# Optimization experiments

Hardware: AMD Instinct MI355X
Metric: run time of the kernel (lower is better)

The kernel has to match this reference:

```python
import jax, jax.numpy as jnp
import numpy as np

B, D, L, E, RH, EH = 8192, 1024, 3, 8, 128, 256  # batch, dim, levels, experts, router hidden, expert hidden


def setup_inputs() -> dict:
    key = jax.random.key(0)
    ks = jax.random.split(key, 9)
    s_d = 1.0 / np.sqrt(D)
    s_rh = 1.0 / np.sqrt(RH)
    s_eh = 1.0 / np.sqrt(EH)
    return {
        "x": jax.random.normal(ks[0], (B, D), dtype=jnp.float32),
        # routers: Linear(D,128) -> ReLU -> Linear(128,E) -> softmax, one per level
        "router_w1": jax.random.uniform(ks[1], (L, D, RH), jnp.float32, -s_d, s_d),
        "router_b1": jax.random.uniform(ks[2], (L, RH), jnp.float32, -s_d, s_d),
        "router_w2": jax.random.uniform(ks[3], (L, RH, E), jnp.float32, -s_rh, s_rh),
        "router_b2": jax.random.uniform(ks[4], (L, E), jnp.float32, -s_rh, s_rh),
        # experts: Linear(D,256) -> ReLU -> Linear(256,D), E per level
        "expert_w1": jax.random.uniform(ks[5], (L, E, D, EH), jnp.float32, -s_d, s_d),
        "expert_b1": jax.random.uniform(ks[6], (L, E, EH), jnp.float32, -s_d, s_d),
        "expert_w2": jax.random.uniform(ks[7], (L, E, EH, D), jnp.float32, -s_eh, s_eh),
        "expert_b2": jax.random.uniform(ks[8], (L, E, D), jnp.float32, -s_eh, s_eh),
    }


def _forward(x, router_w1, router_b1, router_w2, router_b2,
             expert_w1, expert_b1, expert_w2, expert_b2):
    def level(cur, params):
        rw1, rb1, rw2, rb2, ew1, eb1, ew2, eb2 = params
        # router: [B,E] softmax weights
        rh = jax.nn.relu(cur @ rw1 + rb1)
        w = jax.nn.softmax(rh @ rw2 + rb2, axis=-1)
        # dense all-expert eval: grouped GEMMs
        h = jax.nn.relu(jnp.einsum("bd,edh->beh", cur, ew1) + eb1)  # [B,E,EH]
        y = jnp.einsum("beh,ehd->bed", h, ew2) + eb2                # [B,E,D]
        out = jnp.einsum("be,bed->bd", w, y)                        # softmax-weighted sum
        return out, None

    out, _ = jax.lax.scan(
        level, x,
        (router_w1, router_b1, router_w2, router_b2,
         expert_w1, expert_b1, expert_w2, expert_b2))
    return out


def reference(x, router_w1, router_b1, router_w2, router_b2,
              expert_w1, expert_b1, expert_w2, expert_b2):
    return _forward(x, router_w1, router_b1, router_w2, router_b2,
                    expert_w1, expert_b1, expert_w2, expert_b2)
```

## Files before the change

### kernel.cpp

```cpp
#include <hip/hip_runtime.h>
#include <stdint.h>

#define BB   8192
#define DD   1024
#define EE   8
#define RHH  128
#define EHH  256
#define NE1  2048
#define KX   2112

using f32x4  = __attribute__((ext_vector_type(4))) float;
using bf16x8 = __attribute__((ext_vector_type(8))) __bf16;

__device__ __forceinline__ unsigned short f2bf(float f) {
    union { float f; uint32_t u; } v; v.f = f;
    uint32_t u = v.u;
    uint32_t r = (u + 0x7FFFu + ((u >> 16) & 1u)) >> 16;
    return (unsigned short)r;
}
__device__ __forceinline__ float bf2f(unsigned short h) {
    union { uint32_t u; float f; } v; v.u = ((uint32_t)h) << 16;
    return v.f;
}

__device__ __forceinline__ void llds16(void* l, const void* g) {
    __builtin_amdgcn_global_load_lds(
        (const __attribute__((address_space(1))) uint32_t*)g,
        (__attribute__((address_space(3))) uint32_t*)l, 16, 0, 0);
}

__device__ __forceinline__ void rawbar() {
    asm volatile("" ::: "memory");
    __builtin_amdgcn_s_barrier();
    asm volatile("" ::: "memory");
}

template<int N> __device__ __forceinline__ void vmwait() {
    asm volatile("s_waitcnt vmcnt(%0)" :: "n"(N) : "memory");
}

#define MFMA16(a,b,c) __builtin_amdgcn_mfma_f32_16x16x32_bf16(a,b,c,0,0,0)

__device__ __forceinline__ void prep_lvl_body(float (*T)[65], int pbid, int tid,
    const float* __restrict__ rw1, const float* __restrict__ ew1,
    const float* __restrict__ ew2, const float* __restrict__ eb2,
    unsigned short* __restrict__ rw1t, unsigned short* __restrict__ W1t,
    unsigned short* __restrict__ W2t)
{
    const int hl = tid & 63, gq = tid >> 6;
    if (pbid < 512) {
        int e = pbid >> 6, kt = (pbid >> 2) & 15, ht = pbid & 3;
        const float* src = ew1 + ((size_t)e << 18);
#pragma unroll
        for (int i = 0; i < 16; ++i) {
            int kl = i * 4 + gq;
            T[kl][hl] = src[(size_t)(kt * 64 + kl) * 256 + ht * 64 + hl];
        }
        __syncthreads();
#pragma unroll
        for (int i = 0; i < 16; ++i) {
            int hl2 = i * 4 + gq;
            int n = e * 256 + ht * 64 + hl2;
            W1t[(size_t)n * 1024 + kt * 64 + hl] = f2bf(T[hl][hl2]);
        }
    } else if (pbid < 1024) {
        int b2 = pbid - 512;
        int npt = b2 >> 4, dt = b2 & 15;
#pragma unroll
        for (int i = 0; i < 16; ++i) {
            int npl = i * 4 + gq;
            T[npl][hl] = ew2[(size_t)(npt * 64 + npl) * 1024 + dt * 64 + hl];
        }
        __syncthreads();
#pragma unroll
        for (int i = 0; i < 16; ++i) {
            int dl2 = i * 4 + gq;
            int d = dt * 64 + dl2;
            W2t[(size_t)d * KX + npt * 64 + hl] = f2bf(T[hl][dl2]);
        }
    } else if (pbid < 1056) {
        int b2 = pbid - 1024;
        int dt = b2 >> 1, ht = b2 & 1;
#pragma unroll
        for (int i = 0; i < 16; ++i) {
            int dl = i * 4 + gq;
            T[dl][hl] = rw1[(size_t)(dt * 64 + dl) * 128 + ht * 64 + hl];
        }
        __syncthreads();
#pragma unroll
        for (int i = 0; i < 16; ++i) {
            int hl2 = i * 4 + gq;
            int h = ht * 64 + hl2;
            rw1t[(size_t)h * 1024 + dt * 64 + hl] = f2bf(T[hl][hl2]);
        }
    } else if (pbid < 1060) {
        int d = (pbid - 1056) * 256 + tid;
        unsigned short vv[8];
#pragma unroll
        for (int e = 0; e < 8; ++e) vv[e] = f2bf(eb2[(size_t)e * 1024 + d]);
        *(uint4*)&W2t[(size_t)d * KX + NE1] = *(const uint4*)vv;
    } else {
        int d = (pbid - 1060) * 256 + tid;
        uint4 z = make_uint4(0, 0, 0, 0);
#pragma unroll
        for (int j = 0; j < 7; ++j)
            *(uint4*)&W2t[(size_t)d * KX + NE1 + 8 + j * 8] = z;
    }
}

__global__ __launch_bounds__(256) void mega0(
    const float* __restrict__ x, unsigned short* __restrict__ xb,
    unsigned short* __restrict__ Hb,
    const float* __restrict__ rw1, const float* __restrict__ ew1,
    const float* __restrict__ ew2, const float* __restrict__ eb2,
    unsigned short* __restrict__ rw1t, unsigned short* __restrict__ W1t,
    unsigned short* __restrict__ W2t)
{
    __shared__ float T[64][65];
    const int bid = blockIdx.x, tid = threadIdx.x;
    if (bid < 2048) {
        size_t idx = (size_t)bid * 256 + tid;
        const float* p = x + idx * 16;
        uint32_t w[8];
#pragma unroll
        for (int j = 0; j < 8; ++j)
            w[j] = (uint32_t)f2bf(p[2 * j]) | ((uint32_t)f2bf(p[2 * j + 1]) << 16);
        uint32_t* o = (uint32_t*)(xb + idx * 16);
        *(uint4*)(o)     = make_uint4(w[0], w[1], w[2], w[3]);
        *(uint4*)(o + 4) = make_uint4(w[4], w[5], w[6], w[7]);
    } else if (bid < 2080) {
        int row = (bid - 2048) * 256 + tid;
        uint4 z = make_uint4(0, 0, 0, 0);
        unsigned short* p = Hb + (size_t)row * KX + NE1 + EE;
#pragma unroll
        for (int j = 0; j < 7; ++j)
            *(uint4*)(p + j * 8) = z;
    } else {
        prep_lvl_body(T, bid - 2080, tid, rw1, ew1, ew2, eb2, rw1t, W1t, W2t);
    }
}

__global__ __launch_bounds__(256) void prep_lvl(
    const float* __restrict__ rw1, const float* __restrict__ ew1,
    const float* __restrict__ ew2, const float* __restrict__ eb2,
    unsigned short* __restrict__ rw1t, unsigned short* __restrict__ W1t,
    unsigned short* __restrict__ W2t)
{
    __shared__ float T[64][65];
    prep_lvl_body(T, blockIdx.x, threadIdx.x, rw1, ew1, ew2, eb2, rw1t, W1t, W2t);
}

__global__ __launch_bounds__(512, 2) void router_fused(
    const unsigned short* __restrict__ xb, const unsigned short* __restrict__ rw1t,
    const float* __restrict__ rw2, const float* __restrict__ rb1,
    const float* __restrict__ rb2, float* __restrict__ wbuf,
    unsigned short* __restrict__ Hb)
{
    __shared__ __align__(16) char SR[73728];

    const int tid = threadIdx.x;
    const int lane = tid & 63, wv = tid >> 6;
    const int g = wv >> 2, wq = wv & 3;
    const int l16 = lane & 15, lhi = lane >> 4;
    const long m0 = (long)blockIdx.x * 64;

    const int r0 = tid >> 2, sl = tid & 3;
    const int sg = sl ^ ((r0 >> 1) & 3);

    const int xrow = (tid >> 2) & 63, xkg = tid >> 8;
    const char* xsrc = (const char*)xb + (m0 + xrow) * 2048 + xkg * 1024 + sg * 16;
    const char* wsrc = (const char*)rw1t + (long)r0 * 2048 + sg * 16;

    f32x4 acc[8];
    const f32x4 zero = {0.f, 0.f, 0.f, 0.f};
#pragma unroll
    for (int i = 0; i < 8; ++i) acc[i] = zero;

    auto stage = [&](int buf, int t) {
        char* base = SR + buf * 24576;
        llds16(base + tid * 16, xsrc + t * 64);
        llds16(base + 8192 + tid * 16, wsrc + t * 64);
        llds16(base + 16384 + tid * 16, wsrc + 1024 + t * 64);
    };

    stage(0, 0); stage(1, 1);

    const int swz = (l16 >> 1) & 3;
    const int aoff = g * 2048 + (wq * 16 + l16) * 32 + ((lhi ^ swz) << 3);
    const int boff = 4096 + g * 4096 + l16 * 32 + ((lhi ^ swz) << 3);

    int cb = 0, sb = 2;
    for (int t = 0; t < 16; ++t) {
        if (t < 15) vmwait<3>(); else vmwait<0>();
        rawbar();
        const unsigned short* bufp = (const unsigned short*)(SR + cb * 24576);
        bf16x8 aF = *(const bf16x8*)&bufp[aoff];
        bf16x8 bF[8];
#pragma unroll
        for (int ni = 0; ni < 8; ++ni)
            bF[ni] = *(const bf16x8*)&bufp[boff + ni * 512];
        if (t + 2 < 16) stage(sb, t + 2);
        __builtin_amdgcn_s_setprio(1);
#pragma unroll
        for (int ni = 0; ni < 8; ++ni)
            acc[ni] = MFMA16(aF, bF[ni], acc[ni]);
        __builtin_amdgcn_s_setprio(0);
        cb = (cb + 1 == 3) ? 0 : cb + 1;
        sb = (sb + 1 == 3) ? 0 : sb + 1;
    }

    rawbar();

    float* rhs = (float*)SR;
    float* lg  = (float*)(SR + 64 * 132 * 4);

    if (g == 1) {
#pragma unroll
        for (int ni = 0; ni < 8; ++ni)
#pragma unroll
            for (int rr = 0; rr < 4; ++rr)
                rhs[(wq * 16 + lhi * 4 + rr) * 132 + ni * 16 + l16] = acc[ni][rr];
    }
    rawbar();
    if (g == 0) {
#pragma unroll
        for (int ni = 0; ni < 8; ++ni) {
            float bv = rb1[ni * 16 + l16];
#pragma unroll
            for (int rr = 0; rr < 4; ++rr) {
                int row = wq * 16 + lhi * 4 + rr, col = ni * 16 + l16;
                float v = acc[ni][rr] + rhs[row * 132 + col] + bv;
                rhs[row * 132 + col] = fmaxf(v, 0.f);
            }
        }
    }
    rawbar();

    {
        const int row = tid & 63, e = tid >> 6;
        float a2 = rb2[e];
        for (int h = 0; h < 128; ++h)
            a2 += rhs[row * 132 + h] * rw2[h * 8 + e];
        lg[row * 9 + e] = a2;
    }
    rawbar();

    if (tid < 64) {
        const int row = tid;
        float l[8], m = -1e30f;
#pragma unroll
        for (int e = 0; e < 8; ++e) { l[e] = lg[row * 9 + e]; m = fmaxf(m, l[e]); }
        float s = 0.f;
#pragma unroll
        for (int e = 0; e < 8; ++e) { l[e] = expf(l[e] - m); s += l[e]; }
        float inv = 1.f / s;
        const long gr = m0 + row;
#pragma unroll
        for (int e = 0; e < 8; ++e) {
            float w = l[e] * inv;
            wbuf[gr * 8 + e] = w;
            Hb[gr * KX + NE1 + e] = f2bf(w);
        }
    }
}

template<int BNv, int BKv, int NBUF, int WNv, int EPI>
__global__ __launch_bounds__(512, 2)
void gemmT(const unsigned short* __restrict__ A, const unsigned short* __restrict__ Bt,
           void* __restrict__ C, const float* __restrict__ bias,
           const float* __restrict__ wrow,
           int K, int lda, int ldb, int ldc)
{
    constexpr int KH  = BKv / 32;
    constexpr int WMv = 8 / WNv;
    constexpr int MR  = 256 / WMv;
    constexpr int NC  = BNv / WNv;
    constexpr int MI  = MR / 16;
    constexpr int NI  = NC / 16;
    constexpr int NCH = 16 / MI;
    constexpr int ALP = 2;
    constexpr int BLP = (BNv * 64) / 8192;
    constexpr int LPT = KH * (ALP + BLP);
    constexpr int SD  = NBUF - 1;
    constexpr int AKH = 256 * 32;
    constexpr int BKH = BNv * 32;

    __shared__ __align__(16) unsigned short As[NBUF * KH * AKH];
    __shared__ __align__(16) unsigned short Bs[NBUF * KH * BKH];

    const int tid = threadIdx.x;
    const int lane = tid & 63, wv = tid >> 6;
    const int wr = wv / WNv, wc = wv % WNv;
    const int l16 = lane & 15, lhi = lane >> 4;
    const long bm0 = (long)blockIdx.x * 256;
    const long bn0 = (long)blockIdx.y * BNv;

    const int r0 = tid >> 2, sl = tid & 3;
    const int sg = sl ^ ((r0 >> 1) & 3);

    const char* aSrc[ALP];
    const char* bSrc[BLP];
#pragma unroll
    for (int a = 0; a < ALP; ++a)
        aSrc[a] = (const char*)A + (bm0 + a * 128 + r0) * (long)lda * 2 + sg * 16;
#pragma unroll
    for (int b = 0; b < BLP; ++b)
        bSrc[b] = (const char*)Bt + (bn0 + b * 128 + r0) * (long)ldb * 2 + sg * 16;

    f32x4 acc[MI][NI];
    const f32x4 zero = {0.f, 0.f, 0.f, 0.f};
#pragma unroll
    for (int i = 0; i < MI; ++i)
#pragma unroll
        for (int j = 0; j < NI; ++j)
            acc[i][j] = zero;

    auto stage = [&](int buf, int t) {
        const int cbyte = t * (BKv * 2);
#pragma unroll
        for (int kh = 0; kh < KH; ++kh) {
            char* ad = (char*)As + ((buf * KH + kh) * AKH) * 2 + tid * 16;
            char* bd = (char*)Bs + ((buf * KH + kh) * BKH) * 2 + tid * 16;
#pragma unroll
            for (int a = 0; a < ALP; ++a)
                llds16(ad + a * 8192, aSrc[a] + cbyte + kh * 64);
#pragma unroll
            for (int b = 0; b < BLP; ++b)
                llds16(bd + b * 8192, bSrc[b] + cbyte + kh * 64);
        }
    };

    const int nt = K / BKv;
#pragma unroll
    for (int p = 0; p < SD; ++p) stage(p, p);

    const int swz = (l16 >> 1) & 3;
    const int aoff = (wr * MR + l16) * 32 + ((lhi ^ swz) << 3);
    const int boff = (wc * NC + l16) * 32 + ((lhi ^ swz) << 3);

    int cb = 0, sb = SD % NBUF;
    for (int t = 0; t < nt; ++t) {
        const int rem = nt - 1 - t;
        if (rem >= SD - 1) vmwait<LPT * (SD - 1)>();
        else if constexpr (SD >= 3) {
            if (rem == 1) vmwait<LPT>(); else vmwait<0>();
        } else vmwait<0>();
        rawbar();

        bf16x8 aF[KH][MI], bF[KH][NI];
#pragma unroll
        for (int kh = 0; kh < KH; ++kh) {
            const unsigned short* ap = &As[(cb * KH + kh) * AKH];
            const unsigned short* bp = &Bs[(cb * KH + kh) * BKH];
#pragma unroll
            for (int mi = 0; mi < MI; ++mi)
                aF[kh][mi] = *(const bf16x8*)&ap[aoff + mi * 512];
#pragma unroll
            for (int ni = 0; ni < NI; ++ni)
                bF[kh][ni] = *(const bf16x8*)&bp[boff + ni * 512];
        }

        if (t + SD < nt) stage(sb, t + SD);

#pragma unroll
        for (int kh = 0; kh < KH; ++kh) {
#pragma unroll
            for (int nc0 = 0; nc0 < NI; nc0 += NCH) {
                __builtin_amdgcn_s_setprio(1);
#pragma unroll
                for (int mi = 0; mi < MI; ++mi)
#pragma unroll
                    for (int nj = 0; nj < NCH; ++nj)
                        acc[mi][nc0 + nj] = MFMA16(aF[kh][mi], bF[kh][nc0 + nj],
                                                   acc[mi][nc0 + nj]);
                __builtin_amdgcn_s_setprio(0);
            }
        }

        cb = (cb + 1 == NBUF) ? 0 : cb + 1;
        sb = (sb + 1 == NBUF) ? 0 : sb + 1;
    }

#pragma unroll
    for (int mi = 0; mi < MI; ++mi) {
#pragma unroll
        for (int ni = 0; ni < NI; ++ni) {
            const long gn = bn0 + wc * NC + ni * 16 + l16;
            float bv = 0.f;
            if (EPI == 1) bv = bias[gn];
#pragma unroll
            for (int rr = 0; rr < 4; ++rr) {
                const long gm = bm0 + wr * MR + mi * 16 + lhi * 4 + rr;
                float v = acc[mi][ni][rr];
                if (EPI == 1) {
                    v = fmaxf(v + bv, 0.f) * wrow[gm * 8 + (int)(gn >> 8)];
                    ((unsigned short*)C)[gm * (long)ldc + gn] = f2bf(v);
                } else if (EPI == 2) {
                    ((unsigned short*)C)[gm * (long)ldc + gn] = f2bf(v);
                } else {
                    ((float*)C)[gm * (long)ldc + gn] = v;
                }
            }
        }
    }
}


extern "C" void kernel_launch(void* const* d_in, const int* in_sizes, int n_in,
                              void* d_out, int out_size, void* d_ws, size_t ws_size,
                              hipStream_t stream) {
    (void)in_sizes; (void)n_in; (void)out_size; (void)ws_size;
    const float* x   = (const float*)d_in[0];
    const float* rw1 = (const float*)d_in[1];
    const float* rb1 = (const float*)d_in[2];
    const float* rw2 = (const float*)d_in[3];
    const float* rb2 = (const float*)d_in[4];
    const float* ew1 = (const float*)d_in[5];
    const float* eb1 = (const float*)d_in[6];
    const float* ew2 = (const float*)d_in[7];
    const float* eb2 = (const float*)d_in[8];

    char* ws = (char*)d_ws;
    unsigned short* xb   = (unsigned short*)(ws);
    float*          wbuf = (float*)         (ws + 16777216);
    unsigned short* Hb   = (unsigned short*)(ws + 17039360);
    unsigned short* rw1t = (unsigned short*)(ws + 51642368);
    unsigned short* W1t  = (unsigned short*)(ws + 51904512);
    unsigned short* W2t  = (unsigned short*)(ws + 56098816);

    mega0<<<3144, 256, 0, stream>>>(x, xb, Hb, rw1, ew1, ew2, eb2, rw1t, W1t, W2t);

    for (int l = 0; l < 3; ++l) {
        if (l > 0)
            prep_lvl<<<1064, 256, 0, stream>>>(rw1 + (size_t)l * DD * RHH,
                                               ew1 + (size_t)l * EE * DD * EHH,
                                               ew2 + (size_t)l * EE * EHH * DD,
                                               eb2 + (size_t)l * EE * DD,
                                               rw1t, W1t, W2t);

        router_fused<<<128, 512, 0, stream>>>(xb, rw1t,
                                              rw2 + (size_t)l * RHH * EE,
                                              rb1 + (size_t)l * RHH,
                                              rb2 + (size_t)l * EE, wbuf, Hb);

        gemmT<256, 32, 4, 4, 1><<<dim3(32, 8), 512, 0, stream>>>(
            xb, W1t, Hb, eb1 + (size_t)l * NE1, wbuf, DD, DD, DD, KX);

        if (l < 2)
            gemmT<128, 64, 3, 2, 2><<<dim3(32, 8), 512, 0, stream>>>(
                Hb, W2t, xb, nullptr, nullptr, KX, KX, KX, DD);
        else
            gemmT<128, 64, 3, 2, 3><<<dim3(32, 8), 512, 0, stream>>>(
                Hb, W2t, d_out, nullptr, nullptr, KX, KX, KX, DD);
    }
}
```

Before: 281.8 us.

## Double-buffer weight prep and fuse next-level prep into router kernel

Double-buffers the transposed bf16 weight buffers when the workspace is large enough, so the next level's weight transpose/convert runs as extra blocks inside the router kernel instead of as a separate prep launch. This removes one launch per level and overlaps the small router work with weight preparation. Prep and conversion blocks are also widened to 512 threads, and the GEMM grids are flattened to 1D with row-major block ordering, which changes which blocks are co-resident and so their L2 reuse of A and B tiles. It needs extra workspace and falls back to the old path when the workspace is too small.

```diff
diff --git a/kernel.cpp b/kernel.cpp
--- a/kernel.cpp
+++ b/kernel.cpp
@@ -41,7 +41,7 @@
 
 #define MFMA16(a,b,c) __builtin_amdgcn_mfma_f32_16x16x32_bf16(a,b,c,0,0,0)
 
-__device__ __forceinline__ void prep_lvl_body(float (*T)[65], int pbid, int tid,
+__device__ __forceinline__ void prep512(float (*T)[65], int pbid, int tid,
     const float* __restrict__ rw1, const float* __restrict__ ew1,
     const float* __restrict__ ew2, const float* __restrict__ eb2,
     unsigned short* __restrict__ rw1t, unsigned short* __restrict__ W1t,
@@ -52,14 +52,14 @@
         int e = pbid >> 6, kt = (pbid >> 2) & 15, ht = pbid & 3;
         const float* src = ew1 + ((size_t)e << 18);
 #pragma unroll
-        for (int i = 0; i < 16; ++i) {
-            int kl = i * 4 + gq;
+        for (int i = 0; i < 8; ++i) {
+            int kl = i * 8 + gq;
             T[kl][hl] = src[(size_t)(kt * 64 + kl) * 256 + ht * 64 + hl];
         }
         __syncthreads();
 #pragma unroll
-        for (int i = 0; i < 16; ++i) {
-            int hl2 = i * 4 + gq;
+        for (int i = 0; i < 8; ++i) {
+            int hl2 = i * 8 + gq;
             int n = e * 256 + ht * 64 + hl2;
             W1t[(size_t)n * 1024 + kt * 64 + hl] = f2bf(T[hl][hl2]);
         }
@@ -67,14 +67,14 @@
         int b2 = pbid - 512;
         int npt = b2 >> 4, dt = b2 & 15;
 #pragma unroll
-        for (int i = 0; i < 16; ++i) {
-            int npl = i * 4 + gq;
+        for (int i = 0; i < 8; ++i) {
+            int npl = i * 8 + gq;
             T[npl][hl] = ew2[(size_t)(npt * 64 + npl) * 1024 + dt * 64 + hl];
         }
         __syncthreads();
 #pragma unroll
-        for (int i = 0; i < 16; ++i) {
-            int dl2 = i * 4 + gq;
+        for (int i = 0; i < 8; ++i) {
+            int dl2 = i * 8 + gq;
             int d = dt * 64 + dl2;
             W2t[(size_t)d * KX + npt * 64 + hl] = f2bf(T[hl][dl2]);
         }
@@ -82,25 +82,25 @@
         int b2 = pbid - 1024;
         int dt = b2 >> 1, ht = b2 & 1;
 #pragma unroll
-        for (int i = 0; i < 16; ++i) {
-            int dl = i * 4 + gq;
+        for (int i = 0; i < 8; ++i) {
+            int dl = i * 8 + gq;
             T[dl][hl] = rw1[(size_t)(dt * 64 + dl) * 128 + ht * 64 + hl];
         }
         __syncthreads();
 #pragma unroll
-        for (int i = 0; i < 16; ++i) {
-            int hl2 = i * 4 + gq;
+        for (int i = 0; i < 8; ++i) {
+            int hl2 = i * 8 + gq;
             int h = ht * 64 + hl2;
             rw1t[(size_t)h * 1024 + dt * 64 + hl] = f2bf(T[hl][hl2]);
         }
-    } else if (pbid < 1060) {
-        int d = (pbid - 1056) * 256 + tid;
+    } else if (pbid < 1058) {
+        int d = (pbid - 1056) * 512 + tid;
         unsigned short vv[8];
 #pragma unroll
         for (int e = 0; e < 8; ++e) vv[e] = f2bf(eb2[(size_t)e * 1024 + d]);
         *(uint4*)&W2t[(size_t)d * KX + NE1] = *(const uint4*)vv;
     } else {
-        int d = (pbid - 1060) * 256 + tid;
+        int d = (pbid - 1058) * 512 + tid;
         uint4 z = make_uint4(0, 0, 0, 0);
 #pragma unroll
         for (int j = 0; j < 7; ++j)
@@ -108,7 +108,7 @@
     }
 }
 
-__global__ __launch_bounds__(256) void mega0(
+__global__ __launch_bounds__(512) void mega0(
     const float* __restrict__ x, unsigned short* __restrict__ xb,
     unsigned short* __restrict__ Hb,
     const float* __restrict__ rw1, const float* __restrict__ ew1,
@@ -119,50 +119,59 @@
     __shared__ float T[64][65];
     const int bid = blockIdx.x, tid = threadIdx.x;
     if (bid < 2048) {
-        size_t idx = (size_t)bid * 256 + tid;
-        const float* p = x + idx * 16;
-        uint32_t w[8];
-#pragma unroll
-        for (int j = 0; j < 8; ++j)
+        size_t idx = (size_t)bid * 512 + tid;
+        const float* p = x + idx * 8;
+        uint32_t w[4];
+#pragma unroll
+        for (int j = 0; j < 4; ++j)
             w[j] = (uint32_t)f2bf(p[2 * j]) | ((uint32_t)f2bf(p[2 * j + 1]) << 16);
-        uint32_t* o = (uint32_t*)(xb + idx * 16);
-        *(uint4*)(o)     = make_uint4(w[0], w[1], w[2], w[3]);
-        *(uint4*)(o + 4) = make_uint4(w[4], w[5], w[6], w[7]);
-    } else if (bid < 2080) {
-        int row = (bid - 2048) * 256 + tid;
+        *(uint4*)(xb + idx * 8) = make_uint4(w[0], w[1], w[2], w[3]);
+    } else if (bid < 2064) {
+        int row = (bid - 2048) * 512 + tid;
         uint4 z = make_uint4(0, 0, 0, 0);
         unsigned short* p = Hb + (size_t)row * KX + NE1 + EE;
 #pragma unroll
         for (int j = 0; j < 7; ++j)
             *(uint4*)(p + j * 8) = z;
     } else {
-        prep_lvl_body(T, bid - 2080, tid, rw1, ew1, ew2, eb2, rw1t, W1t, W2t);
-    }
-}
-
-__global__ __launch_bounds__(256) void prep_lvl(
+        prep512(T, bid - 2064, tid, rw1, ew1, ew2, eb2, rw1t, W1t, W2t);
+    }
+}
+
+__global__ __launch_bounds__(512) void prep_lvl512(
     const float* __restrict__ rw1, const float* __restrict__ ew1,
     const float* __restrict__ ew2, const float* __restrict__ eb2,
     unsigned short* __restrict__ rw1t, unsigned short* __restrict__ W1t,
     unsigned short* __restrict__ W2t)
 {
     __shared__ float T[64][65];
-    prep_lvl_body(T, blockIdx.x, threadIdx.x, rw1, ew1, ew2, eb2, rw1t, W1t, W2t);
-}
-
-__global__ __launch_bounds__(512, 2) void router_fused(
+    prep512(T, blockIdx.x, threadIdx.x, rw1, ew1, ew2, eb2, rw1t, W1t, W2t);
+}
+
+__global__ __launch_bounds__(512, 2) void router_prep(
     const unsigned short* __restrict__ xb, const unsigned short* __restrict__ rw1t,
     const float* __restrict__ rw2, const float* __restrict__ rb1,
     const float* __restrict__ rb2, float* __restrict__ wbuf,
-    unsigned short* __restrict__ Hb)
+    unsigned short* __restrict__ Hb,
+    const float* __restrict__ rw1_n, const float* __restrict__ ew1_n,
+    const float* __restrict__ ew2_n, const float* __restrict__ eb2_n,
+    unsigned short* __restrict__ rw1t_n, unsigned short* __restrict__ W1t_n,
+    unsigned short* __restrict__ W2t_n)
 {
     __shared__ __align__(16) char SR[73728];
-
+    const int bid = blockIdx.x;
     const int tid = threadIdx.x;
+
+    if (bid >= 128) {
+        prep512((float (*)[65])SR, bid - 128, tid, rw1_n, ew1_n, ew2_n, eb2_n,
+                rw1t_n, W1t_n, W2t_n);
+        return;
+    }
+
     const int lane = tid & 63, wv = tid >> 6;
     const int g = wv >> 2, wq = wv & 3;
     const int l16 = lane & 15, lhi = lane >> 4;
-    const long m0 = (long)blockIdx.x * 64;
+    const long m0 = (long)bid * 64;
 
     const int r0 = tid >> 2, sl = tid & 3;
     const int sg = sl ^ ((r0 >> 1) & 3);
@@ -292,8 +301,9 @@
     const int lane = tid & 63, wv = tid >> 6;
     const int wr = wv / WNv, wc = wv % WNv;
     const int l16 = lane & 15, lhi = lane >> 4;
-    const long bm0 = (long)blockIdx.x * 256;
-    const long bn0 = (long)blockIdx.y * BNv;
+    const int bid = blockIdx.x;
+    const long bm0 = (long)(bid >> 3) * 256;
+    const long bn0 = (long)(bid & 7) * BNv;
 
     const int r0 = tid >> 2, sl = tid & 3;
     const int sg = sl ^ ((r0 >> 1) & 3);
@@ -409,7 +419,7 @@
 extern "C" void kernel_launch(void* const* d_in, const int* in_sizes, int n_in,
                               void* d_out, int out_size, void* d_ws, size_t ws_size,
                               hipStream_t stream) {
-    (void)in_sizes; (void)n_in; (void)out_size; (void)ws_size;
+    (void)in_sizes; (void)n_in; (void)out_size;
     const float* x   = (const float*)d_in[0];
     const float* rw1 = (const float*)d_in[1];
     const float* rb1 = (const float*)d_in[2];
@@ -420,37 +430,57 @@
     const float* ew2 = (const float*)d_in[7];
     const float* eb2 = (const float*)d_in[8];
 
+    const bool dbuf = ws_size >= 69206016u;
+
     char* ws = (char*)d_ws;
     unsigned short* xb   = (unsigned short*)(ws);
     float*          wbuf = (float*)         (ws + 16777216);
     unsigned short* Hb   = (unsigned short*)(ws + 17039360);
-    unsigned short* rw1t = (unsigned short*)(ws + 51642368);
-    unsigned short* W1t  = (unsigned short*)(ws + 51904512);
-    unsigned short* W2t  = (unsigned short*)(ws + 56098816);
-
-    mega0<<<3144, 256, 0, stream>>>(x, xb, Hb, rw1, ew1, ew2, eb2, rw1t, W1t, W2t);
+    size_t off = 51642368;
+    unsigned short* rw1tb[2];
+    unsigned short* W1tb[2];
+    unsigned short* W2tb[2];
+    rw1tb[0] = (unsigned short*)(ws + off);
+    rw1tb[1] = dbuf ? (unsigned short*)(ws + off + 262144) : rw1tb[0];
+    off += (dbuf ? 2u : 1u) * 262144u;
+    W1tb[0] = (unsigned short*)(ws + off);
+    W1tb[1] = dbuf ? (unsigned short*)(ws + off + 4194304) : W1tb[0];
+    off += (dbuf ? 2u : 1u) * 4194304u;
+    W2tb[0] = (unsigned short*)(ws + off);
+    W2tb[1] = dbuf ? (unsigned short*)(ws + off + 4325376) : W2tb[0];
+
+    mega0<<<3124, 512, 0, stream>>>(x, xb, Hb, rw1, ew1, ew2, eb2,
+                                    rw1tb[0], W1tb[0], W2tb[0]);
 
     for (int l = 0; l < 3; ++l) {
-        if (l > 0)
-            prep_lvl<<<1064, 256, 0, stream>>>(rw1 + (size_t)l * DD * RHH,
-                                               ew1 + (size_t)l * EE * DD * EHH,
-                                               ew2 + (size_t)l * EE * EHH * DD,
-                                               eb2 + (size_t)l * EE * DD,
-                                               rw1t, W1t, W2t);
-
-        router_fused<<<128, 512, 0, stream>>>(xb, rw1t,
-                                              rw2 + (size_t)l * RHH * EE,
-                                              rb1 + (size_t)l * RHH,
-                                              rb2 + (size_t)l * EE, wbuf, Hb);
-
-        gemmT<256, 32, 4, 4, 1><<<dim3(32, 8), 512, 0, stream>>>(
-            xb, W1t, Hb, eb1 + (size_t)l * NE1, wbuf, DD, DD, DD, KX);
+        const int b  = dbuf ? (l & 1) : 0;
+        const int nb = dbuf ? (b ^ 1) : 0;
+        const int ln = (l + 1 < 3) ? (l + 1) : 0;
+
+        if (!dbuf && l > 0)
+            prep_lvl512<<<1060, 512, 0, stream>>>(rw1 + (size_t)l * DD * RHH,
+                                                  ew1 + (size_t)l * EE * DD * EHH,
+                                                  ew2 + (size_t)l * EE * EHH * DD,
+                                                  eb2 + (size_t)l * EE * DD,
+                                                  rw1tb[0], W1tb[0], W2tb[0]);
+
+        const int rp_grid = (dbuf && l < 2) ? 1188 : 128;
+        router_prep<<<rp_grid, 512, 0, stream>>>(
+            xb, rw1tb[b],
+            rw2 + (size_t)l * RHH * EE, rb1 + (size_t)l * RHH, rb2 + (size_t)l * EE,
+            wbuf, Hb,
+            rw1 + (size_t)ln * DD * RHH, ew1 + (size_t)ln * EE * DD * EHH,
+            ew2 + (size_t)ln * EE * EHH * DD, eb2 + (size_t)ln * EE * DD,
+            rw1tb[nb], W1tb[nb], W2tb[nb]);
+
+        gemmT<256, 32, 4, 4, 1><<<256, 512, 0, stream>>>(
+            xb, W1tb[b], Hb, eb1 + (size_t)l * NE1, wbuf, DD, DD, DD, KX);
 
         if (l < 2)
-            gemmT<128, 64, 3, 2, 2><<<dim3(32, 8), 512, 0, stream>>>(
-                Hb, W2t, xb, nullptr, nullptr, KX, KX, KX, DD);
+            gemmT<128, 64, 3, 2, 2><<<256, 512, 0, stream>>>(
+                Hb, W2tb[b], xb, nullptr, nullptr, KX, KX, KX, DD);
         else
-            gemmT<128, 64, 3, 2, 3><<<dim3(32, 8), 512, 0, stream>>>(
-                Hb, W2t, d_out, nullptr, nullptr, KX, KX, KX, DD);
-    }
-}
+            gemmT<128, 64, 3, 2, 3><<<256, 512, 0, stream>>>(
+                Hb, W2tb[b], d_out, nullptr, nullptr, KX, KX, KX, DD);
+    }
+}
```

New measurement: 300.0 us. 6.5% more time.
